# Optimization experiments

Measured on AMD Instinct MI355X. Metric: run time of the kernel, lower is better.

The kernel has to match this reference:

```python
import jax, jax.numpy as jnp
import numpy as np

B, T, IN, H, L = 256, 80, 39, 256, 5


def _xavier(key, shape):
    fan_out, fan_in = shape[0], shape[1]
    std = (2.0 / (fan_in + fan_out)) ** 0.5
    return std * jax.random.normal(key, shape, dtype=jnp.float32)


def setup_inputs() -> dict:
    key = jax.random.key(0)
    ks = jax.random.split(key, 4 + 2 * L)
    x = jax.random.normal(ks[0], (B, T, IN), dtype=jnp.float32)
    # PyTorch LSTM params, gate order (i, f, g, o); biases zero per init.
    W_ih0 = _xavier(ks[1], (4 * H, IN))                       # layer 0 input weights
    W_ih_rest = jnp.stack([_xavier(ks[2 + l], (4 * H, H)) for l in range(L - 1)])  # [L-1,4H,H]
    W_hh = jnp.stack([_xavier(ks[1 + L + l], (4 * H, H)) for l in range(L)])       # [L,4H,H]
    b_ih = jnp.zeros((L, 4 * H), dtype=jnp.float32)
    b_hh = jnp.zeros((L, 4 * H), dtype=jnp.float32)
    fc_w = _xavier(ks[2 * L + 1], (1, H))
    fc_b = jnp.zeros((1,), dtype=jnp.float32)
    return {"x": x, "W_ih0": W_ih0, "W_ih_rest": W_ih_rest, "W_hh": W_hh,
            "b_ih": b_ih, "b_hh": b_hh, "fc_w": fc_w, "fc_b": fc_b}


def _lstm_layer(xs, W_ih, W_hh_l, b_ih_l, b_hh_l):
    # xs: [B,T,D]. Precompute input projection for all timesteps (one big GEMM).
    x_proj = jnp.einsum('btd,gd->btg', xs, W_ih) + b_ih_l + b_hh_l  # [B,T,4H]

    def step(carry, xp):
        h, c = carry
        gates = xp + h @ W_hh_l.T                 # [B,4H]
        i, f, g, o = jnp.split(gates, 4, axis=-1)
        c = jax.nn.sigmoid(f) * c + jax.nn.sigmoid(i) * jnp.tanh(g)
        h = jax.nn.sigmoid(o) * jnp.tanh(c)
        return (h, c), h

    b = xs.shape[0]
    h0 = jnp.zeros((b, H), dtype=xs.dtype)
    _, hs = jax.lax.scan(step, (h0, h0), jnp.swapaxes(x_proj, 0, 1))
    return jnp.swapaxes(hs, 0, 1)  # [B,T,H]


def reference(x, W_ih0, W_ih_rest, W_hh, b_ih, b_hh, fc_w, fc_b):
    h = _lstm_layer(x, W_ih0, W_hh[0], b_ih[0], b_hh[0])
    for l in range(1, L):
        h = _lstm_layer(h, W_ih_rest[l - 1], W_hh[l], b_ih[l], b_hh[l])
    out = jnp.einsum('bth,oh->bto', h, fc_w) + fc_b  # [B,T,1]
    return out[..., 0]  # [B,T]
```

## Files before the change

kernel.cpp:

```cpp
#include <hip/hip_runtime.h>

#define B_ 256
#define T_ 80
#define IN_ 39
#define H_ 256
#define G_ 1024
#define L_ 5
#define TC_ 16
#define NCH_ 5

#define XP_FLOATS   (B_ * TC_ * G_)
#define HBUF_FLOATS (B_ * T_ * H_)
#define CBUF_FLOATS (B_ * H_)
#define WG_FLOATS   (L_ * G_ * H_)
#define HX_FLOATS   (2 * 32 * 2048)
#define CNT_OFF_FLOATS (XP_FLOATS + HBUF_FLOATS + CBUF_FLOATS + WG_FLOATS + HX_FLOATS)

#define AG __HIP_MEMORY_SCOPE_AGENT

__device__ __forceinline__ float sigm(float x) { return 1.0f / (1.0f + expf(-x)); }
__device__ __forceinline__ void fma4(float4& a, float s, const float4& w) {
    a.x = fmaf(s, w.x, a.x); a.y = fmaf(s, w.y, a.y);
    a.z = fmaf(s, w.z, a.z); a.w = fmaf(s, w.w, a.w);
}
__device__ __forceinline__ void red4(float4& a) {
    a.x += __shfl_xor(a.x, 32); a.y += __shfl_xor(a.y, 32);
    a.z += __shfl_xor(a.z, 32); a.w += __shfl_xor(a.w, 32);
}
__device__ __forceinline__ float lo32(unsigned long long v) { return __uint_as_float((unsigned)v); }
__device__ __forceinline__ float hi32(unsigned long long v) { return __uint_as_float((unsigned)(v >> 32)); }

extern "C" __global__ void __launch_bounds__(256)
wt_kernel(const float* __restrict__ Whh, float* __restrict__ Wg) {
    const int gid = blockIdx.x * 256 + threadIdx.x;
    const int g4 = gid & 3;
    const int j  = (gid >> 2) & 31;
    const int k  = (gid >> 7) & 255;
    const int s  = (gid >> 15) & 7;
    const int l  = gid >> 18;
    Wg[gid] = Whh[((size_t)(l * 1024 + g4 * 256 + s * 32 + j)) * 256 + k];
}

extern "C" __global__ void __launch_bounds__(256)
proj_kernel(const float* __restrict__ src, const float* __restrict__ Wih,
            const float* __restrict__ bihl, const float* __restrict__ bhhl,
            float* __restrict__ xp, int K, int t0) {
    __shared__ float As[16 * 68];
    __shared__ float Bs[16 * 68];
    const int tid = threadIdx.x;
    const int mt = blockIdx.x >> 4, nt = blockIdx.x & 15;
    const int tx = tid & 15, ty = tid >> 4;
    const int lr = tid >> 2, lc4 = (tid & 3) << 2;

    const int ar = mt * 64 + lr;
    const int ab = ar >> 4;
    const int at = t0 + (ar & 15);
    const float* arow = src + ((size_t)ab * T_ + at) * K;
    const float* brow = Wih + (size_t)(nt * 64 + lr) * K;

    float acc[4][4];
    #pragma unroll
    for (int i = 0; i < 4; ++i)
        #pragma unroll
        for (int j = 0; j < 4; ++j) acc[i][j] = 0.0f;

    for (int k0 = 0; k0 < K; k0 += 16) {
        __syncthreads();
        if (K == IN_) {
            #pragma unroll
            for (int i = 0; i < 4; ++i) {
                int k = k0 + lc4 + i;
                As[(lc4 + i) * 68 + lr] = (k < IN_) ? arow[k] : 0.0f;
                Bs[(lc4 + i) * 68 + lr] = (k < IN_) ? brow[k] : 0.0f;
            }
        } else {
            float4 av = *(const float4*)(arow + k0 + lc4);
            float4 bv = *(const float4*)(brow + k0 + lc4);
            As[(lc4 + 0) * 68 + lr] = av.x;
            As[(lc4 + 1) * 68 + lr] = av.y;
            As[(lc4 + 2) * 68 + lr] = av.z;
            As[(lc4 + 3) * 68 + lr] = av.w;
            Bs[(lc4 + 0) * 68 + lr] = bv.x;
            Bs[(lc4 + 1) * 68 + lr] = bv.y;
            Bs[(lc4 + 2) * 68 + lr] = bv.z;
            Bs[(lc4 + 3) * 68 + lr] = bv.w;
        }
        __syncthreads();
        #pragma unroll
        for (int kk = 0; kk < 16; ++kk) {
            float4 a4 = *(const float4*)&As[kk * 68 + ty * 4];
            float4 b4 = *(const float4*)&Bs[kk * 68 + tx * 4];
            acc[0][0] += a4.x * b4.x; acc[0][1] += a4.x * b4.y;
            acc[0][2] += a4.x * b4.z; acc[0][3] += a4.x * b4.w;
            acc[1][0] += a4.y * b4.x; acc[1][1] += a4.y * b4.y;
            acc[1][2] += a4.y * b4.z; acc[1][3] += a4.y * b4.w;
            acc[2][0] += a4.z * b4.x; acc[2][1] += a4.z * b4.y;
            acc[2][2] += a4.z * b4.z; acc[2][3] += a4.z * b4.w;
            acc[3][0] += a4.w * b4.x; acc[3][1] += a4.w * b4.y;
            acc[3][2] += a4.w * b4.z; acc[3][3] += a4.w * b4.w;
        }
    }
    const int col = nt * 64 + tx * 4;
    const float bs0 = bihl[col + 0] + bhhl[col + 0];
    const float bs1 = bihl[col + 1] + bhhl[col + 1];
    const float bs2 = bihl[col + 2] + bhhl[col + 2];
    const float bs3 = bihl[col + 3] + bhhl[col + 3];
    #pragma unroll
    for (int i = 0; i < 4; ++i) {
        const int row = mt * 64 + ty * 4 + i;
        float4 o;
        o.x = acc[i][0] + bs0; o.y = acc[i][1] + bs1;
        o.z = acc[i][2] + bs2; o.w = acc[i][3] + bs3;
        *(float4*)&xp[(size_t)row * G_ + col] = o;
    }
}

extern "C" __global__ void __launch_bounds__(512, 2)
rec3_kernel(const float* __restrict__ xp, const float* __restrict__ Wg_l,
            float* __restrict__ hbuf, float* __restrict__ cbuf,
            float* __restrict__ hx, int* __restrict__ cnt,
            int t0, int chkb, int first) {
    __shared__ float sH[2048];
    __shared__ float sP[8 * 32 * 36];

    const int tid = threadIdx.x;
    const int bid = blockIdx.x;
    const int grp = bid & 31;
    const int s   = bid >> 5;
    const int jj  = tid & 31;
    const int ks  = tid >> 5;
    const int w   = tid >> 6;
    const int fb  = (tid >> 5) & 7;
    const int fj  = tid & 31;
    const int bglob = grp * 8 + fb;
    const int unit  = s * 32 + fj;
    int* cnt_g = cnt + grp * 32;

    const float4* Wg4 = (const float4*)Wg_l + (size_t)s * 8192;
    float4 wreg[16];
    #pragma unroll
    for (int kk = 0; kk < 16; ++kk)
        wreg[kk] = Wg4[(size_t)(ks * 16 + kk) * 32 + jj];

    float creg = 0.0f;
    if (tid < 256 && !first) creg = cbuf[(size_t)bglob * H_ + unit];

    const float4* sH4 = (const float4*)sH;

    for (int tt = 0; tt < TC_; ++tt) {
        const int t = t0 + tt;

        if (tt == 0) {
            if (first) {
                for (int i = tid; i < 2048; i += 512) sH[i] = 0.0f;
            } else if (tid < 256) {
                const int u = tid;
                #pragma unroll
                for (int bb = 0; bb < 8; ++bb)
                    sH[u * 8 + bb] = hbuf[((size_t)(grp * 8 + bb) * T_ + (t0 - 1)) * H_ + u];
            }
        } else {
            if (tid == 0) {
                const int tgt = 8 * (chkb + tt);
                while (__hip_atomic_load(cnt_g, __ATOMIC_RELAXED, AG) < tgt)
                    __builtin_amdgcn_s_sleep(1);
            }
            __syncthreads();
            if (tid < 256) {
                const unsigned long long* hs =
                    (const unsigned long long*)(hx + (size_t)(((tt - 1) & 1) * 32 + grp) * 2048);
                const int u = tid;
                unsigned long long v0 = __hip_atomic_load(hs + u * 4 + 0, __ATOMIC_RELAXED, AG);
                unsigned long long v1 = __hip_atomic_load(hs + u * 4 + 1, __ATOMIC_RELAXED, AG);
                unsigned long long v2 = __hip_atomic_load(hs + u * 4 + 2, __ATOMIC_RELAXED, AG);
                unsigned long long v3 = __hip_atomic_load(hs + u * 4 + 3, __ATOMIC_RELAXED, AG);
                float4 fa, fbv;
                fa.x = lo32(v0); fa.y = hi32(v0); fa.z = lo32(v1); fa.w = hi32(v1);
                fbv.x = lo32(v2); fbv.y = hi32(v2); fbv.z = lo32(v3); fbv.w = hi32(v3);
                *(float4*)&sH[u * 8] = fa;
                *(float4*)&sH[u * 8 + 4] = fbv;
            }
        }

        float x0 = 0.f, x1 = 0.f, x2 = 0.f, x3 = 0.f;
        if (tid < 256) {
            const size_t xrow = ((size_t)bglob * TC_ + tt) * G_ + unit;
            x0 = xp[xrow];
            x1 = xp[xrow + 256];
            x2 = xp[xrow + 512];
            x3 = xp[xrow + 768];
        }

        __syncthreads();

        float4 a0 = {0,0,0,0}, a1 = {0,0,0,0}, a2 = {0,0,0,0}, a3 = {0,0,0,0};
        float4 a4 = {0,0,0,0}, a5 = {0,0,0,0}, a6 = {0,0,0,0}, a7 = {0,0,0,0};
        #pragma unroll
        for (int kk = 0; kk < 16; ++kk) {
            const int k = ks * 16 + kk;
            const float4 wv = wreg[kk];
            const float4 ha = sH4[k * 2];
            const float4 hb = sH4[k * 2 + 1];
            fma4(a0, ha.x, wv); fma4(a1, ha.y, wv);
            fma4(a2, ha.z, wv); fma4(a3, ha.w, wv);
            fma4(a4, hb.x, wv); fma4(a5, hb.y, wv);
            fma4(a6, hb.z, wv); fma4(a7, hb.w, wv);
        }
        red4(a0); red4(a1); red4(a2); red4(a3);
        red4(a4); red4(a5); red4(a6); red4(a7);
        if ((tid & 63) < 32) {
            float4* pp = (float4*)&sP[(w * 32 + jj) * 36];
            pp[0] = a0; pp[1] = a1; pp[2] = a2; pp[3] = a3;
            pp[4] = a4; pp[5] = a5; pp[6] = a6; pp[7] = a7;
        }
        __syncthreads();

        if (tid < 256) {
            float4 g4;
            g4.x = x0; g4.y = x1; g4.z = x2; g4.w = x3;
            #pragma unroll
            for (int w2 = 0; w2 < 8; ++w2) {
                const float4 pw = *(const float4*)&sP[(w2 * 32 + fj) * 36 + fb * 4];
                g4.x += pw.x; g4.y += pw.y; g4.z += pw.z; g4.w += pw.w;
            }
            const float I = sigm(g4.x);
            const float F = sigm(g4.y);
            const float Gt = tanhf(g4.z);
            const float O = sigm(g4.w);
            creg = F * creg + I * Gt;
            const float hval = O * tanhf(creg);
            hbuf[((size_t)bglob * T_ + t) * H_ + unit] = hval;

            if (tt < TC_ - 1) {
                __hip_atomic_store(hx + (size_t)((tt & 1) * 32 + grp) * 2048 + unit * 8 + fb,
                                   hval, __ATOMIC_RELAXED, AG);
            }
        }

        if (tt < TC_ - 1) {
            asm volatile("s_waitcnt vmcnt(0)" ::: "memory");
            __syncthreads();
            if (tid == 0)
                __hip_atomic_fetch_add(cnt_g, 1, __ATOMIC_RELAXED, AG);
        }
    }

    if (tid < 256) cbuf[(size_t)bglob * H_ + unit] = creg;
}

extern "C" __global__ void __launch_bounds__(128)
fc_kernel(const float* __restrict__ hbuf, const float* __restrict__ fcw,
          const float* __restrict__ fcb, float* __restrict__ out) {
    __shared__ float wsm[256];
    const int tid = threadIdx.x;
    const int b = blockIdx.x;
    if (tid < 64) ((float4*)wsm)[tid] = ((const float4*)fcw)[tid];
    __syncthreads();
    if (tid < T_) {
        const float4* h4p = (const float4*)(hbuf + ((size_t)b * T_ + tid) * H_);
        const float4* w4p = (const float4*)wsm;
        float acc = fcb[0];
        #pragma unroll 8
        for (int k4 = 0; k4 < 64; ++k4) {
            float4 h4 = h4p[k4], w4 = w4p[k4];
            acc += h4.x * w4.x + h4.y * w4.y + h4.z * w4.z + h4.w * w4.w;
        }
        out[b * T_ + tid] = acc;
    }
}

extern "C" void kernel_launch(void* const* d_in, const int* in_sizes, int n_in,
                              void* d_out, int out_size, void* d_ws, size_t ws_size,
                              hipStream_t stream) {
    (void)in_sizes; (void)n_in; (void)out_size; (void)ws_size;
    const float* x    = (const float*)d_in[0];
    const float* Wih0 = (const float*)d_in[1];
    const float* Wihr = (const float*)d_in[2];
    const float* Whh  = (const float*)d_in[3];
    const float* bih  = (const float*)d_in[4];
    const float* bhh  = (const float*)d_in[5];
    const float* fcw  = (const float*)d_in[6];
    const float* fcb  = (const float*)d_in[7];
    float* out = (float*)d_out;
    float* ws  = (float*)d_ws;

    float* xp   = ws;
    float* hbuf = ws + XP_FLOATS;
    float* cbuf = hbuf + HBUF_FLOATS;
    float* wg   = cbuf + CBUF_FLOATS;
    float* hx   = wg + WG_FLOATS;
    int*   cnt  = (int*)(ws + CNT_OFF_FLOATS);

    hipMemsetAsync(cnt, 0, 32 * 32 * sizeof(int), stream);
    hipLaunchKernelGGL(wt_kernel, dim3(WG_FLOATS / 256), dim3(256), 0, stream, Whh, wg);

    for (int l = 0; l < L_; ++l) {
        const int K = (l == 0) ? IN_ : H_;
        const float* src = (l == 0) ? x : hbuf;
        const float* Wih = (l == 0) ? Wih0 : (Wihr + (size_t)(l - 1) * G_ * H_);
        const float* Wg_l = wg + (size_t)l * (G_ * H_);
        for (int ch = 0; ch < NCH_; ++ch) {
            const int t0 = ch * TC_;
            const int chkb = (l * NCH_ + ch) * (TC_ - 1);
            hipLaunchKernelGGL(proj_kernel, dim3(1024), dim3(256), 0, stream,
                               src, Wih, bih + l * G_, bhh + l * G_, xp, K, t0);
            hipLaunchKernelGGL(rec3_kernel, dim3(256), dim3(512), 0, stream,
                               xp, Wg_l, hbuf, cbuf, hx, cnt, t0, chkb, ch == 0 ? 1 : 0);
        }
    }
    hipLaunchKernelGGL(fc_kernel, dim3(B_), dim3(128), 0, stream, hbuf, fcw, fcb, out);
}
```

Measured before the change: 2.604 ms.

## Fuse next-chunk input projection into the recurrent LSTM kernel

Removes the separate proj_kernel launches for layers 1-4. Each recurrent block now loads a transposed slice of W_ih into registers. After every timestep it computes the input projection for the matching timestep of the next chunk, or of the next layer's first chunk, from hbuf values not yet overwritten. This is meant to cut the launch and serialization cost between projection and recurrence. In exchange it adds projection work and extra barriers inside the latency-bound recurrent loop, and adds register pressure under launch_bounds(512,2).

```diff
diff --git a/kernel.cpp b/kernel.cpp
--- a/kernel.cpp
+++ b/kernel.cpp
@@ -116,11 +116,14 @@
 }
 
 extern "C" __global__ void __launch_bounds__(512, 2)
-rec3_kernel(const float* __restrict__ xp, const float* __restrict__ Wg_l,
+rec4_kernel(float* __restrict__ xp, const float* __restrict__ Wg_l,
             float* __restrict__ hbuf, float* __restrict__ cbuf,
             float* __restrict__ hx, int* __restrict__ cnt,
-            int t0, int chkb, int first) {
+            const float* __restrict__ wih_t, const float* __restrict__ bih_t,
+            const float* __restrict__ bhh_t,
+            int t0, int chkb, int first, int do_proj, int src_t0) {
     __shared__ float sH[2048];
+    __shared__ float sA[2048];
     __shared__ float sP[8 * 32 * 36];
 
     const int tid = threadIdx.x;
@@ -142,10 +145,38 @@
     for (int kk = 0; kk < 16; ++kk)
         wreg[kk] = Wg4[(size_t)(ks * 16 + kk) * 32 + jj];
 
+    float4 wf[16];
+    float pb0 = 0.f, pb1 = 0.f, pb2 = 0.f, pb3 = 0.f;
+    if (do_proj) {
+        const int pj = s * 32 + jj;
+        float4 tg0[4], tg1[4], tg2[4], tg3[4];
+        #pragma unroll
+        for (int c = 0; c < 4; ++c) {
+            tg0[c] = *(const float4*)&wih_t[((size_t)(0 * 256 + pj)) * 256 + ks * 16 + c * 4];
+            tg1[c] = *(const float4*)&wih_t[((size_t)(1 * 256 + pj)) * 256 + ks * 16 + c * 4];
+            tg2[c] = *(const float4*)&wih_t[((size_t)(2 * 256 + pj)) * 256 + ks * 16 + c * 4];
+            tg3[c] = *(const float4*)&wih_t[((size_t)(3 * 256 + pj)) * 256 + ks * 16 + c * 4];
+        }
+        #pragma unroll
+        for (int c = 0; c < 4; ++c) {
+            wf[c * 4 + 0] = make_float4(tg0[c].x, tg1[c].x, tg2[c].x, tg3[c].x);
+            wf[c * 4 + 1] = make_float4(tg0[c].y, tg1[c].y, tg2[c].y, tg3[c].y);
+            wf[c * 4 + 2] = make_float4(tg0[c].z, tg1[c].z, tg2[c].z, tg3[c].z);
+            wf[c * 4 + 3] = make_float4(tg0[c].w, tg1[c].w, tg2[c].w, tg3[c].w);
+        }
+        if (tid < 256) {
+            pb0 = bih_t[0 * 256 + unit] + bhh_t[0 * 256 + unit];
+            pb1 = bih_t[1 * 256 + unit] + bhh_t[1 * 256 + unit];
+            pb2 = bih_t[2 * 256 + unit] + bhh_t[2 * 256 + unit];
+            pb3 = bih_t[3 * 256 + unit] + bhh_t[3 * 256 + unit];
+        }
+    }
+
     float creg = 0.0f;
     if (tid < 256 && !first) creg = cbuf[(size_t)bglob * H_ + unit];
 
     const float4* sH4 = (const float4*)sH;
+    const float4* sA4 = (const float4*)sA;
 
     for (int tt = 0; tt < TC_; ++tt) {
         const int t = t0 + tt;
@@ -230,18 +261,64 @@
             creg = F * creg + I * Gt;
             const float hval = O * tanhf(creg);
             hbuf[((size_t)bglob * T_ + t) * H_ + unit] = hval;
-
             if (tt < TC_ - 1) {
                 __hip_atomic_store(hx + (size_t)((tt & 1) * 32 + grp) * 2048 + unit * 8 + fb,
                                    hval, __ATOMIC_RELAXED, AG);
             }
         }
-
         if (tt < TC_ - 1) {
             asm volatile("s_waitcnt vmcnt(0)" ::: "memory");
             __syncthreads();
             if (tid == 0)
                 __hip_atomic_fetch_add(cnt_g, 1, __ATOMIC_RELAXED, AG);
+        } else if (do_proj) {
+            __syncthreads();
+        }
+
+        if (do_proj) {
+            if (tid < 256) {
+                const int u = tid;
+                #pragma unroll
+                for (int bb = 0; bb < 8; ++bb)
+                    sA[u * 8 + bb] =
+                        hbuf[((size_t)(grp * 8 + bb) * T_ + (src_t0 + tt)) * H_ + u];
+            }
+            __syncthreads();
+            float4 p0 = {0,0,0,0}, p1 = {0,0,0,0}, p2 = {0,0,0,0}, p3 = {0,0,0,0};
+            float4 p4 = {0,0,0,0}, p5 = {0,0,0,0}, p6 = {0,0,0,0}, p7 = {0,0,0,0};
+            #pragma unroll
+            for (int kk = 0; kk < 16; ++kk) {
+                const int k = ks * 16 + kk;
+                const float4 wv = wf[kk];
+                const float4 ha = sA4[k * 2];
+                const float4 hb = sA4[k * 2 + 1];
+                fma4(p0, ha.x, wv); fma4(p1, ha.y, wv);
+                fma4(p2, ha.z, wv); fma4(p3, ha.w, wv);
+                fma4(p4, hb.x, wv); fma4(p5, hb.y, wv);
+                fma4(p6, hb.z, wv); fma4(p7, hb.w, wv);
+            }
+            red4(p0); red4(p1); red4(p2); red4(p3);
+            red4(p4); red4(p5); red4(p6); red4(p7);
+            if ((tid & 63) < 32) {
+                float4* pp = (float4*)&sP[(w * 32 + jj) * 36];
+                pp[0] = p0; pp[1] = p1; pp[2] = p2; pp[3] = p3;
+                pp[4] = p4; pp[5] = p5; pp[6] = p6; pp[7] = p7;
+            }
+            __syncthreads();
+            if (tid < 256) {
+                float4 g4;
+                g4.x = pb0; g4.y = pb1; g4.z = pb2; g4.w = pb3;
+                #pragma unroll
+                for (int w2 = 0; w2 < 8; ++w2) {
+                    const float4 pw = *(const float4*)&sP[(w2 * 32 + fj) * 36 + fb * 4];
+                    g4.x += pw.x; g4.y += pw.y; g4.z += pw.z; g4.w += pw.w;
+                }
+                const size_t xrow = ((size_t)bglob * TC_ + tt) * G_ + unit;
+                xp[xrow]       = g4.x;
+                xp[xrow + 256] = g4.y;
+                xp[xrow + 512] = g4.z;
+                xp[xrow + 768] = g4.w;
+            }
         }
     }
 
@@ -295,17 +372,27 @@
     hipLaunchKernelGGL(wt_kernel, dim3(WG_FLOATS / 256), dim3(256), 0, stream, Whh, wg);
 
     for (int l = 0; l < L_; ++l) {
-        const int K = (l == 0) ? IN_ : H_;
-        const float* src = (l == 0) ? x : hbuf;
-        const float* Wih = (l == 0) ? Wih0 : (Wihr + (size_t)(l - 1) * G_ * H_);
         const float* Wg_l = wg + (size_t)l * (G_ * H_);
         for (int ch = 0; ch < NCH_; ++ch) {
             const int t0 = ch * TC_;
-            const int chkb = (l * NCH_ + ch) * (TC_ - 1);
-            hipLaunchKernelGGL(proj_kernel, dim3(1024), dim3(256), 0, stream,
-                               src, Wih, bih + l * G_, bhh + l * G_, xp, K, t0);
-            hipLaunchKernelGGL(rec3_kernel, dim3(256), dim3(512), 0, stream,
-                               xp, Wg_l, hbuf, cbuf, hx, cnt, t0, chkb, ch == 0 ? 1 : 0);
+            const int gc = l * NCH_ + ch;
+            const int chkb = gc * (TC_ - 1);
+            if (l == 0) {
+                hipLaunchKernelGGL(proj_kernel, dim3(1024), dim3(256), 0, stream,
+                                   x, Wih0, bih, bhh, xp, IN_, t0);
+            }
+            int lt, do_proj;
+            if (ch < NCH_ - 1) { lt = l;     do_proj = (l >= 1) ? 1 : 0; }
+            else               { lt = l + 1; do_proj = (lt <= L_ - 1) ? 1 : 0; }
+            const int ltc = do_proj ? lt : 1;
+            const float* wih_t = Wihr + (size_t)(ltc - 1) * G_ * H_;
+            const float* biht  = bih + ltc * G_;
+            const float* bhht  = bhh + ltc * G_;
+            const int src_t0 = (ch < NCH_ - 1) ? (t0 + TC_) : 0;
+            hipLaunchKernelGGL(rec4_kernel, dim3(256), dim3(512), 0, stream,
+                               xp, Wg_l, hbuf, cbuf, hx, cnt,
+                               wih_t, biht, bhht,
+                               t0, chkb, ch == 0 ? 1 : 0, do_proj, src_t0);
         }
     }
     hipLaunchKernelGGL(fc_kernel, dim3(B_), dim3(128), 0, stream, hbuf, fcw, fcb, out);
```

Measured after the change: 3.425 ms. 31.5% more time.
